# Kernel optimization log

Hardware: AMD Instinct MI355X
Metric: run time of the kernel (lower is better)

## Reference

```python
import jax, jax.numpy as jnp
import numpy as np

N, K = 50000, 16          # nodes, fixed neighbor-list length
IN, HID, OUT = 11, 64, 1  # temporal feat dim, hidden, output


def setup_inputs() -> dict:
    key = jax.random.key(0)
    ks = iter(jax.random.split(key, 64))
    def rn(shape, scale=1.0):
        return jax.random.normal(next(ks), shape, dtype=jnp.float32) * scale
    inp = {
        "x": rn((N, IN)),
        "neighbors": jax.random.randint(next(ks), (N, K), 0, N, dtype=jnp.int32),
        "prev_hidden": rn((N, HID)),
    }
    # DGL SAGEConv(lstm): LSTM(in=d, hid=d), fc_self Linear(d,o,bias=True), fc_neigh Linear(d,o,bias=False)
    dims = [(IN, HID), (HID, HID), (HID, HID), (HID, OUT)]
    for li, (d, o) in enumerate(dims, start=1):
        s = 1.0 / np.sqrt(d)
        inp[f"l{li}_Wih"] = rn((4 * d, d), s)
        inp[f"l{li}_Whh"] = rn((4 * d, d), s)
        inp[f"l{li}_bih"] = rn((4 * d,), s)
        inp[f"l{li}_bhh"] = rn((4 * d,), s)
        inp[f"l{li}_Ws"] = rn((o, d), s)
        inp[f"l{li}_bs"] = rn((o,), s)
        inp[f"l{li}_Wn"] = rn((o, d), s)
    sg = 1.0 / np.sqrt(HID)
    inp["g_Wih"] = rn((3 * HID, HID), sg)
    inp["g_Whh"] = rn((3 * HID, HID), sg)
    inp["g_bih"] = rn((3 * HID,), sg)
    inp["g_bhh"] = rn((3 * HID,), sg)
    return inp


def _sage_conv(h, neighbors, Wih, Whh, bih, bhh, Ws, bs, Wn):
    """DGL SAGEConv with aggregator_type='lstm'."""
    m = h[neighbors]             # [N, K, D] gathered neighbor messages
    ms = jnp.swapaxes(m, 0, 1)   # [K, N, D] time-major for scan
    Nn, D = h.shape
    h0 = jnp.zeros((Nn, D), h.dtype)

    def step(carry, mt):
        hp, cp = carry
        g = mt @ Wih.T + bih + hp @ Whh.T + bhh   # [N, 4D]
        i, f, gg, o = jnp.split(g, 4, axis=-1)    # torch LSTM gate order i,f,g,o
        c = jax.nn.sigmoid(f) * cp + jax.nn.sigmoid(i) * jnp.tanh(gg)
        hn = jax.nn.sigmoid(o) * jnp.tanh(c)
        return (hn, c), None

    (hK, _), _ = jax.lax.scan(step, (h0, h0), ms)  # final hidden state = neighbor agg
    return h @ Ws.T + bs + hK @ Wn.T


def _gru(x, h, Wih, Whh, bih, bhh):
    """torch.nn.GRUCell, gate order r,z,n."""
    gi = x @ Wih.T + bih
    gh = h @ Whh.T + bhh
    ir, iz, inn = jnp.split(gi, 3, axis=-1)
    hr, hz, hn = jnp.split(gh, 3, axis=-1)
    r = jax.nn.sigmoid(ir + hr)
    z = jax.nn.sigmoid(iz + hz)
    n = jnp.tanh(inn + r * hn)
    return (1.0 - z) * n + z * h


def reference(x, neighbors, prev_hidden,
              l1_Wih, l1_Whh, l1_bih, l1_bhh, l1_Ws, l1_bs, l1_Wn,
              l2_Wih, l2_Whh, l2_bih, l2_bhh, l2_Ws, l2_bs, l2_Wn,
              l3_Wih, l3_Whh, l3_bih, l3_bhh, l3_Ws, l3_bs, l3_Wn,
              l4_Wih, l4_Whh, l4_bih, l4_bhh, l4_Ws, l4_bs, l4_Wn,
              g_Wih, g_Whh, g_bih, g_bhh):
    h = jax.nn.relu(_sage_conv(x, neighbors, l1_Wih, l1_Whh, l1_bih, l1_bhh, l1_Ws, l1_bs, l1_Wn))
    h = jax.nn.relu(_sage_conv(h, neighbors, l2_Wih, l2_Whh, l2_bih, l2_bhh, l2_Ws, l2_bs, l2_Wn))
    h = jax.nn.relu(_sage_conv(h, neighbors, l3_Wih, l3_Whh, l3_bih, l3_bhh, l3_Ws, l3_bs, l3_Wn))
    h = _gru(h, prev_hidden, g_Wih, g_Whh, g_bih, g_bhh)
    logits = _sage_conv(h, neighbors, l4_Wih, l4_Whh, l4_bih, l4_bhh, l4_Ws, l4_bs, l4_Wn)
    return logits
```

## Files before the change

### kernel.cpp

```cpp
#include <hip/hip_runtime.h>

#define N_NODES 50000

typedef __bf16 bf16x8 __attribute__((ext_vector_type(8)));
typedef float f32x4 __attribute__((ext_vector_type(4)));

union U16x8 { uint4 v; unsigned short u[8]; bf16x8 b; };

__device__ __forceinline__ float b2f(unsigned short h){
  unsigned int u = ((unsigned int)h) << 16;
  return __builtin_bit_cast(float, u);
}
__device__ __forceinline__ unsigned short f2b(float x){
  unsigned int u = __builtin_bit_cast(unsigned int, x);
  u = u + 0x7FFFu + ((u >> 16) & 1u);
  return (unsigned short)(u >> 16);
}
__device__ __forceinline__ float sigm(float x){
  const float e = __builtin_amdgcn_exp2f(x * -1.4426950408889634f);
  return __builtin_amdgcn_rcpf(1.0f + e);
}
__device__ __forceinline__ float tanh_(float x){
  const float e = __builtin_amdgcn_exp2f(x * 2.8853900817779268f);
  return fmaf(-2.0f, __builtin_amdgcn_rcpf(1.0f + e), 1.0f);
}

__device__ __forceinline__ bf16x8 load8_bf16(const float* p){
  float4 a = *(const float4*)p; float4 c = *(const float4*)(p + 4);
  U16x8 r;
  r.u[0]=f2b(a.x); r.u[1]=f2b(a.y); r.u[2]=f2b(a.z); r.u[3]=f2b(a.w);
  r.u[4]=f2b(c.x); r.u[5]=f2b(c.y); r.u[6]=f2b(c.z); r.u[7]=f2b(c.w);
  return r.b;
}


__global__ __launch_bounds__(256) void l1_kernel(
    const float* __restrict__ x, const int* __restrict__ nbr,
    const float* __restrict__ Wih, const float* __restrict__ Whh,
    const float* __restrict__ bih, const float* __restrict__ bhh,
    const float* __restrict__ Ws,  const float* __restrict__ bs,
    const float* __restrict__ Wn,  unsigned short* __restrict__ out_hl)
{
  __shared__ unsigned short mbuf[16][2][16][24];
  __shared__ unsigned short hbuf[2][2][16][24];
  __shared__ float pre[4][16][17];

  const int tid  = threadIdx.x;
  const int wave = tid >> 6, lane = tid & 63;
  const int n16  = lane & 15, q = lane >> 4;
  const int nb0  = blockIdx.x * 16;

  { unsigned int* p = (unsigned int*)hbuf;
    for (int i = tid; i < 768; i += 256) p[i] = 0u; }

  {
    const int nd = tid >> 4, t = tid & 15;
    const int gn = nbr[(nb0 + nd) * 16 + t];
    const float* row = x + (long)gn * 11;
    float v[16];
    #pragma unroll
    for (int j = 0; j < 11; j++) v[j] = row[j];
    #pragma unroll
    for (int j = 11; j < 16; j++) v[j] = 0.f;
    #pragma unroll
    for (int j = 0; j < 16; j++){
      unsigned short hb = f2b(v[j]);
      mbuf[t][0][nd][j] = hb;
      mbuf[t][1][nd][j] = f2b(v[j] - b2f(hb));
    }
  }

  bf16x8 wf;
  {
    const int u = n16;
    const float* src = (q < 2) ? (Wih + (wave * 11 + u) * 11)
                               : (Whh + (wave * 11 + u) * 11);
    const int kb = (q & 1) * 8;
    U16x8 a;
    #pragma unroll
    for (int j = 0; j < 8; j++){
      const int k = kb + j;
      float v = (u < 11 && k < 11) ? src[k] : 0.f;
      a.u[j] = f2b(v);
    }
    wf = a.b;
  }
  const float bg = (n16 < 11) ? (bih[wave * 11 + n16] + bhh[wave * 11 + n16]) : 0.f;

  const int nd_o = tid & 15, u_o = tid >> 4;
  float c_o = 0.f;

  __syncthreads();

  for (int t = 0; t < 16; t++){
    const int db = t & 1, nb = db ^ 1;

    const unsigned short* ph = (q < 2) ? &mbuf[t][0][n16][q * 8]
                                       : &hbuf[db][0][n16][(q - 2) * 8];
    U16x8 ah, al;
    ah.v = *(const uint4*)ph;
    al.v = *(const uint4*)(ph + 384);

    f32x4 acc = {bg, bg, bg, bg};
    acc = __builtin_amdgcn_mfma_f32_16x16x32_bf16(ah.b, wf, acc, 0, 0, 0);
    acc = __builtin_amdgcn_mfma_f32_16x16x32_bf16(al.b, wf, acc, 0, 0, 0);

    #pragma unroll
    for (int r = 0; r < 4; r++) pre[wave][q * 4 + r][n16] = acc[r];
    __syncthreads();

    if (tid < 176){
      const float gi = pre[0][nd_o][u_o];
      const float gf = pre[1][nd_o][u_o];
      const float gg = pre[2][nd_o][u_o];
      const float go = pre[3][nd_o][u_o];
      c_o = sigm(gf) * c_o + sigm(gi) * tanh_(gg);
      const float hv = sigm(go) * tanh_(c_o);
      const unsigned short hb = f2b(hv);
      hbuf[nb][0][nd_o][u_o] = hb;
      hbuf[nb][1][nd_o][u_o] = f2b(hv - b2f(hb));
    }
    __syncthreads();
  }

  U16x8 eah, eal;
  if (q < 2){
    const float* row = x + (long)(nb0 + n16) * 11;
    U16x8 H, L;
    #pragma unroll
    for (int j = 0; j < 8; j++){
      const int k = q * 8 + j;
      float v = (k < 11) ? row[k] : 0.f;
      unsigned short hb = f2b(v); H.u[j] = hb; L.u[j] = f2b(v - b2f(hb));
    }
    eah = H; eal = L;
  } else {
    const unsigned short* ph = &hbuf[0][0][n16][(q - 2) * 8];
    eah.v = *(const uint4*)ph;
    eal.v = *(const uint4*)(ph + 384);
  }

  bf16x8 ewf;
  {
    const int uo = wave * 16 + n16;
    const float* src = (q < 2) ? (Ws + uo * 11) : (Wn + uo * 11);
    const int kb = (q & 1) * 8;
    U16x8 a;
    #pragma unroll
    for (int j = 0; j < 8; j++){
      const int k = kb + j;
      a.u[j] = f2b((k < 11) ? src[k] : 0.f);
    }
    ewf = a.b;
  }

  {
    const int uo = wave * 16 + n16;
    const float bsv = bs[uo];
    f32x4 e = {bsv, bsv, bsv, bsv};
    e = __builtin_amdgcn_mfma_f32_16x16x32_bf16(eah.b, ewf, e, 0, 0, 0);
    e = __builtin_amdgcn_mfma_f32_16x16x32_bf16(eal.b, ewf, e, 0, 0, 0);
    #pragma unroll
    for (int r = 0; r < 4; r++){
      const float vv = fmaxf(e[r], 0.f);
      const unsigned short hb = f2b(vv);
      const size_t base = (size_t)(nb0 + q * 4 + r) * 128;
      out_hl[base + uo]      = hb;
      out_hl[base + 64 + uo] = f2b(vv - b2f(hb));
    }
  }
}

__global__ __launch_bounds__(256, 3) void sage64_kernel(
    const unsigned short* __restrict__ in_hl, const int* __restrict__ nbr,
    const float* __restrict__ Wih, const float* __restrict__ Whh,
    const float* __restrict__ bih, const float* __restrict__ bhh,
    const float* __restrict__ Ws,  const float* __restrict__ bs,
    const float* __restrict__ Wn,
    unsigned short* __restrict__ out_hl, float* __restrict__ out_f32, int mode)
{
  __shared__ uint4 mbuf[2][16][17];
  __shared__ uint4 hbuf[2][16][17];
  __shared__ int nbr_s[16 * 17];

  const int tid = threadIdx.x;
  const int wv = tid >> 6, lane = tid & 63;
  const int n16 = lane & 15, q = lane >> 4;
  const int nb0 = blockIdx.x * 16;

  { const int nd = tid >> 4, t = tid & 15;
    nbr_s[nd * 17 + t] = nbr[(nb0 + nd) * 16 + t]; }

  { unsigned int* p = (unsigned int*)&hbuf[0][0][0];
    for (int i = tid; i < 1088; i += 256) p[i] = 0u; }

  { const int nd = tid >> 4, s = tid & 15;
    const int gn = nbr[(nb0 + nd) * 16 + 0];
    mbuf[0][nd][s] = *(const uint4*)(in_hl + (size_t)gn * 128 + s * 8); }

  bf16x8 wih_f[4][2], whh_f[4][2];
  #pragma unroll
  for (int g = 0; g < 4; g++){
    const int row = g * 64 + wv * 16 + n16;
    #pragma unroll
    for (int kc = 0; kc < 2; kc++){
      wih_f[g][kc] = load8_bf16(Wih + row * 64 + kc * 32 + q * 8);
      whh_f[g][kc] = load8_bf16(Whh + row * 64 + kc * 32 + q * 8);
    }
  }
  f32x4 bg[4];
  #pragma unroll
  for (int g = 0; g < 4; g++){
    float4 bi = *(const float4*)(bih + g * 64 + wv * 16 + q * 4);
    float4 bh = *(const float4*)(bhh + g * 64 + wv * 16 + q * 4);
    f32x4 s = {bi.x + bh.x, bi.y + bh.y, bi.z + bh.z, bi.w + bh.w};
    bg[g] = s;
  }

  float c4[4] = {0.f, 0.f, 0.f, 0.f};
  __syncthreads();

  for (int t = 0; t < 16; t++){
    const int db = t & 1, nbf = db ^ 1;

    bf16x8 mh[2], ml[2], hh[2], hl[2];
    #pragma unroll
    for (int kc = 0; kc < 2; kc++){
      U16x8 a; a.v = mbuf[db][n16][kc * 4 + q];     mh[kc] = a.b;
      U16x8 b_; b_.v = mbuf[db][n16][8 + kc * 4 + q]; ml[kc] = b_.b;
      U16x8 c_; c_.v = hbuf[db][n16][kc * 4 + q];     hh[kc] = c_.b;
      U16x8 d_; d_.v = hbuf[db][n16][8 + kc * 4 + q]; hl[kc] = d_.b;
    }

    uint4 gv = make_uint4(0u, 0u, 0u, 0u);
    const int nd = tid >> 4, s = tid & 15;
    if (t < 15){
      const int gn = nbr_s[nd * 17 + t + 1];
      gv = *(const uint4*)(in_hl + (size_t)gn * 128 + s * 8);
    }

    f32x4 acc[4];
    #pragma unroll
    for (int g = 0; g < 4; g++) acc[g] = bg[g];
    #pragma unroll
    for (int kc = 0; kc < 2; kc++){
      #pragma unroll
      for (int g = 0; g < 4; g++)
        acc[g] = __builtin_amdgcn_mfma_f32_16x16x32_bf16(wih_f[g][kc], mh[kc], acc[g], 0, 0, 0);
      #pragma unroll
      for (int g = 0; g < 4; g++)
        acc[g] = __builtin_amdgcn_mfma_f32_16x16x32_bf16(wih_f[g][kc], ml[kc], acc[g], 0, 0, 0);
      #pragma unroll
      for (int g = 0; g < 4; g++)
        acc[g] = __builtin_amdgcn_mfma_f32_16x16x32_bf16(whh_f[g][kc], hh[kc], acc[g], 0, 0, 0);
      #pragma unroll
      for (int g = 0; g < 4; g++)
        acc[g] = __builtin_amdgcn_mfma_f32_16x16x32_bf16(whh_f[g][kc], hl[kc], acc[g], 0, 0, 0);
    }

    unsigned short hB[4], lB[4];
    #pragma unroll
    for (int r = 0; r < 4; r++){
      const float iv = sigm(acc[0][r]);
      const float fv = sigm(acc[1][r]);
      const float gg = tanh_(acc[2][r]);
      const float ov = sigm(acc[3][r]);
      c4[r] = fv * c4[r] + iv * gg;
      const float hv = ov * tanh_(c4[r]);
      hB[r] = f2b(hv);
      lB[r] = f2b(hv - b2f(hB[r]));
    }
    {
      uint2* hrow = (uint2*)&hbuf[nbf][n16][0];
      hrow[wv * 4 + q]      = make_uint2((unsigned)hB[0] | ((unsigned)hB[1] << 16),
                                         (unsigned)hB[2] | ((unsigned)hB[3] << 16));
      hrow[16 + wv * 4 + q] = make_uint2((unsigned)lB[0] | ((unsigned)lB[1] << 16),
                                         (unsigned)lB[2] | ((unsigned)lB[3] << 16));
    }
    if (t < 15) mbuf[nbf][nd][s] = gv;
    __syncthreads();
  }

  bf16x8 sH[2], sL[2], kH[2], kL[2];
  #pragma unroll
  for (int kc = 0; kc < 2; kc++){
    U16x8 a; a.v = *(const uint4*)(in_hl + (size_t)(nb0 + n16) * 128 + kc * 32 + q * 8);
    sH[kc] = a.b;
    U16x8 b_; b_.v = *(const uint4*)(in_hl + (size_t)(nb0 + n16) * 128 + 64 + kc * 32 + q * 8);
    sL[kc] = b_.b;
    U16x8 c_; c_.v = hbuf[0][n16][kc * 4 + q];     kH[kc] = c_.b;
    U16x8 d_; d_.v = hbuf[0][n16][8 + kc * 4 + q]; kL[kc] = d_.b;
  }

  if (mode == 0){
    bf16x8 ws_f[2], wn_f[2];
    #pragma unroll
    for (int kc = 0; kc < 2; kc++){
      ws_f[kc] = load8_bf16(Ws + (wv * 16 + n16) * 64 + kc * 32 + q * 8);
      wn_f[kc] = load8_bf16(Wn + (wv * 16 + n16) * 64 + kc * 32 + q * 8);
    }
    float4 bsv = *(const float4*)(bs + wv * 16 + q * 4);
    f32x4 e = {bsv.x, bsv.y, bsv.z, bsv.w};
    #pragma unroll
    for (int kc = 0; kc < 2; kc++){
      e = __builtin_amdgcn_mfma_f32_16x16x32_bf16(ws_f[kc], sH[kc], e, 0, 0, 0);
      e = __builtin_amdgcn_mfma_f32_16x16x32_bf16(ws_f[kc], sL[kc], e, 0, 0, 0);
      e = __builtin_amdgcn_mfma_f32_16x16x32_bf16(wn_f[kc], kH[kc], e, 0, 0, 0);
      e = __builtin_amdgcn_mfma_f32_16x16x32_bf16(wn_f[kc], kL[kc], e, 0, 0, 0);
    }
    unsigned short hB[4], lB[4];
    #pragma unroll
    for (int r = 0; r < 4; r++){
      const float vv = fmaxf(e[r], 0.f);
      hB[r] = f2b(vv);
      lB[r] = f2b(vv - b2f(hB[r]));
    }
    uint2* orow = (uint2*)(out_hl + (size_t)(nb0 + n16) * 128);
    orow[wv * 4 + q]      = make_uint2((unsigned)hB[0] | ((unsigned)hB[1] << 16),
                                       (unsigned)hB[2] | ((unsigned)hB[3] << 16));
    orow[16 + wv * 4 + q] = make_uint2((unsigned)lB[0] | ((unsigned)lB[1] << 16),
                                       (unsigned)lB[2] | ((unsigned)lB[3] << 16));
  } else {
    if (wv == 0){
      bf16x8 ws_f[2], wn_f[2];
      #pragma unroll
      for (int kc = 0; kc < 2; kc++){
        U16x8 a, b_;
        a.v = make_uint4(0u,0u,0u,0u); b_.v = make_uint4(0u,0u,0u,0u);
        if (n16 == 0){
          a.b  = load8_bf16(Ws + kc * 32 + q * 8);
          b_.b = load8_bf16(Wn + kc * 32 + q * 8);
        }
        ws_f[kc] = a.b; wn_f[kc] = b_.b;
      }
      f32x4 e = {0.f, 0.f, 0.f, 0.f};
      #pragma unroll
      for (int kc = 0; kc < 2; kc++){
        e = __builtin_amdgcn_mfma_f32_16x16x32_bf16(ws_f[kc], sH[kc], e, 0, 0, 0);
        e = __builtin_amdgcn_mfma_f32_16x16x32_bf16(ws_f[kc], sL[kc], e, 0, 0, 0);
        e = __builtin_amdgcn_mfma_f32_16x16x32_bf16(wn_f[kc], kH[kc], e, 0, 0, 0);
        e = __builtin_amdgcn_mfma_f32_16x16x32_bf16(wn_f[kc], kL[kc], e, 0, 0, 0);
      }
      if (q == 0) out_f32[nb0 + n16] = e[0] + bs[0];
    }
  }
}

__global__ __launch_bounds__(256) void gru_kernel(
    const unsigned short* __restrict__ h3_hl, const float* __restrict__ prev,
    const float* __restrict__ gWih, const float* __restrict__ gWhh,
    const float* __restrict__ gbih, const float* __restrict__ gbhh,
    unsigned short* __restrict__ out_hl)
{
  const int tid = threadIdx.x, wave = tid >> 6, lane = tid & 63;
  const int n16 = lane & 15, q = lane >> 4;
  const int nb0 = blockIdx.x * 16;
  const int u_ = wave * 16 + n16;

  bf16x8 ah[2], al[2], ap[2];
  #pragma unroll
  for (int kc = 0; kc < 2; kc++){
    U16x8 a; a.v = *(const uint4*)(h3_hl + (size_t)(nb0 + n16) * 128 + kc * 32 + q * 8);
    ah[kc] = a.b;
    U16x8 b_; b_.v = *(const uint4*)(h3_hl + (size_t)(nb0 + n16) * 128 + 64 + kc * 32 + q * 8);
    al[kc] = b_.b;
    ap[kc] = load8_bf16(prev + (size_t)(nb0 + n16) * 64 + kc * 32 + q * 8);
  }

  bf16x8 wi_f[3][2], wh_f[3][2];
  #pragma unroll
  for (int g = 0; g < 3; g++){
    const int row = g * 64 + wave * 16 + n16;
    #pragma unroll
    for (int kc = 0; kc < 2; kc++){
      wi_f[g][kc] = load8_bf16(gWih + row * 64 + kc * 32 + q * 8);
      wh_f[g][kc] = load8_bf16(gWhh + row * 64 + kc * 32 + q * 8);
    }
  }

  f32x4 gi[3], gh[3];
  #pragma unroll
  for (int g = 0; g < 3; g++){
    const float bi = gbih[g * 64 + u_], bh = gbhh[g * 64 + u_];
    f32x4 vi = {bi, bi, bi, bi}; gi[g] = vi;
    f32x4 vh = {bh, bh, bh, bh}; gh[g] = vh;
  }
  #pragma unroll
  for (int kc = 0; kc < 2; kc++){
    #pragma unroll
    for (int g = 0; g < 3; g++)
      gi[g] = __builtin_amdgcn_mfma_f32_16x16x32_bf16(ah[kc], wi_f[g][kc], gi[g], 0, 0, 0);
    #pragma unroll
    for (int g = 0; g < 3; g++)
      gi[g] = __builtin_amdgcn_mfma_f32_16x16x32_bf16(al[kc], wi_f[g][kc], gi[g], 0, 0, 0);
    #pragma unroll
    for (int g = 0; g < 3; g++)
      gh[g] = __builtin_amdgcn_mfma_f32_16x16x32_bf16(ap[kc], wh_f[g][kc], gh[g], 0, 0, 0);
  }

  #pragma unroll
  for (int r = 0; r < 4; r++){
    const long node = nb0 + q * 4 + r;
    const float rv = sigm(gi[0][r] + gh[0][r]);
    const float zv = sigm(gi[1][r] + gh[1][r]);
    const float nv = tanh_(gi[2][r] + rv * gh[2][r]);
    const float hp = prev[node * 64 + u_];
    const float v = (1.f - zv) * nv + zv * hp;
    const unsigned short hb = f2b(v);
    out_hl[(size_t)node * 128 + u_]      = hb;
    out_hl[(size_t)node * 128 + 64 + u_] = f2b(v - b2f(hb));
  }
}

extern "C" void kernel_launch(void* const* d_in, const int* in_sizes, int n_in,
                              void* d_out, int out_size, void* d_ws, size_t ws_size,
                              hipStream_t stream)
{
  (void)in_sizes; (void)n_in; (void)out_size; (void)ws_size;
  const float* x    = (const float*)d_in[0];
  const int*   nbr  = (const int*)d_in[1];
  const float* prev = (const float*)d_in[2];
  auto W = [&](int i){ return (const float*)d_in[i]; };

  unsigned short* tabA = (unsigned short*)d_ws;
  unsigned short* tabB = tabA + (size_t)N_NODES * 128;

  l1_kernel<<<N_NODES / 16, 256, 0, stream>>>(
      x, nbr, W(3), W(4), W(5), W(6), W(7), W(8), W(9), tabA);
  sage64_kernel<<<N_NODES / 16, 256, 0, stream>>>(
      tabA, nbr, W(10), W(11), W(12), W(13), W(14), W(15), W(16), tabB, nullptr, 0);
  sage64_kernel<<<N_NODES / 16, 256, 0, stream>>>(
      tabB, nbr, W(17), W(18), W(19), W(20), W(21), W(22), W(23), tabA, nullptr, 0);
  gru_kernel<<<N_NODES / 16, 256, 0, stream>>>(
      tabA, prev, W(31), W(32), W(33), W(34), tabB);
  sage64_kernel<<<N_NODES / 16, 256, 0, stream>>>(
      tabB, nbr, W(24), W(25), W(26), W(27), W(28), W(29), W(30),
      nullptr, (float*)d_out, 1);
}
```

Before: 598.5 us.

## Drop bf16 hi/lo split activations, prefetch all neighbors to LDS up front

Stores intermediate activations as a single bf16 value instead of a hi+lo bf16 pair, which halves gather traffic and halves the number of MFMAs per LSTM step and in the GRU and projection stages. The sage64 kernel now loads all 16 neighbor rows into shared memory with an XOR-style swizzle before the recurrence, replacing the per-step double-buffered gather. Occupancy hint rises from 3 to 4 blocks. Accuracy drops because the lo correction term is gone, which may exceed tolerance for the deep LSTM chain.

```diff
diff --git a/kernel.cpp b/kernel.cpp
--- a/kernel.cpp
+++ b/kernel.cpp
@@ -163,15 +163,12 @@
     #pragma unroll
     for (int r = 0; r < 4; r++){
       const float vv = fmaxf(e[r], 0.f);
-      const unsigned short hb = f2b(vv);
-      const size_t base = (size_t)(nb0 + q * 4 + r) * 128;
-      out_hl[base + uo]      = hb;
-      out_hl[base + 64 + uo] = f2b(vv - b2f(hb));
-    }
-  }
-}
-
-__global__ __launch_bounds__(256, 3) void sage64_kernel(
+      out_hl[(size_t)(nb0 + q * 4 + r) * 64 + uo] = f2b(vv);
+    }
+  }
+}
+
+__global__ __launch_bounds__(256, 4) void sage64_kernel(
     const unsigned short* __restrict__ in_hl, const int* __restrict__ nbr,
     const float* __restrict__ Wih, const float* __restrict__ Whh,
     const float* __restrict__ bih, const float* __restrict__ bhh,
@@ -179,24 +176,24 @@
     const float* __restrict__ Wn,
     unsigned short* __restrict__ out_hl, float* __restrict__ out_f32, int mode)
 {
-  __shared__ uint4 mbuf[2][16][17];
-  __shared__ uint4 hbuf[2][16][17];
-  __shared__ int nbr_s[16 * 17];
+  __shared__ uint4 mbuf[16][16][8];
+  __shared__ uint4 hbuf[2][16][8];
 
   const int tid = threadIdx.x;
   const int wv = tid >> 6, lane = tid & 63;
   const int n16 = lane & 15, q = lane >> 4;
   const int nb0 = blockIdx.x * 16;
 
-  { const int nd = tid >> 4, t = tid & 15;
-    nbr_s[nd * 17 + t] = nbr[(nb0 + nd) * 16 + t]; }
-
+  {
+    const int nd = tid >> 4, t = tid & 15;
+    const int gn = nbr[(nb0 + nd) * 16 + t];
+    const uint4* src = (const uint4*)(in_hl + (size_t)gn * 64);
+    #pragma unroll
+    for (int s = 0; s < 8; s++)
+      mbuf[t][nd][(s + nd + t) & 7] = src[s];
+  }
   { unsigned int* p = (unsigned int*)&hbuf[0][0][0];
-    for (int i = tid; i < 1088; i += 256) p[i] = 0u; }
-
-  { const int nd = tid >> 4, s = tid & 15;
-    const int gn = nbr[(nb0 + nd) * 16 + 0];
-    mbuf[0][nd][s] = *(const uint4*)(in_hl + (size_t)gn * 128 + s * 8); }
+    for (int i = tid; i < 512; i += 256) p[i] = 0u; }
 
   bf16x8 wih_f[4][2], whh_f[4][2];
   #pragma unroll
@@ -223,20 +220,11 @@
   for (int t = 0; t < 16; t++){
     const int db = t & 1, nbf = db ^ 1;
 
-    bf16x8 mh[2], ml[2], hh[2], hl[2];
-    #pragma unroll
-    for (int kc = 0; kc < 2; kc++){
-      U16x8 a; a.v = mbuf[db][n16][kc * 4 + q];     mh[kc] = a.b;
-      U16x8 b_; b_.v = mbuf[db][n16][8 + kc * 4 + q]; ml[kc] = b_.b;
-      U16x8 c_; c_.v = hbuf[db][n16][kc * 4 + q];     hh[kc] = c_.b;
-      U16x8 d_; d_.v = hbuf[db][n16][8 + kc * 4 + q]; hl[kc] = d_.b;
-    }
-
-    uint4 gv = make_uint4(0u, 0u, 0u, 0u);
-    const int nd = tid >> 4, s = tid & 15;
-    if (t < 15){
-      const int gn = nbr_s[nd * 17 + t + 1];
-      gv = *(const uint4*)(in_hl + (size_t)gn * 128 + s * 8);
+    bf16x8 mh[2], hh[2];
+    #pragma unroll
+    for (int kc = 0; kc < 2; kc++){
+      U16x8 a; a.v = mbuf[t][n16][(kc * 4 + q + n16 + t) & 7]; mh[kc] = a.b;
+      U16x8 c_; c_.v = hbuf[db][n16][(kc * 4 + q + n16) & 7];  hh[kc] = c_.b;
     }
 
     f32x4 acc[4];
@@ -249,16 +237,10 @@
         acc[g] = __builtin_amdgcn_mfma_f32_16x16x32_bf16(wih_f[g][kc], mh[kc], acc[g], 0, 0, 0);
       #pragma unroll
       for (int g = 0; g < 4; g++)
-        acc[g] = __builtin_amdgcn_mfma_f32_16x16x32_bf16(wih_f[g][kc], ml[kc], acc[g], 0, 0, 0);
-      #pragma unroll
-      for (int g = 0; g < 4; g++)
         acc[g] = __builtin_amdgcn_mfma_f32_16x16x32_bf16(whh_f[g][kc], hh[kc], acc[g], 0, 0, 0);
-      #pragma unroll
-      for (int g = 0; g < 4; g++)
-        acc[g] = __builtin_amdgcn_mfma_f32_16x16x32_bf16(whh_f[g][kc], hl[kc], acc[g], 0, 0, 0);
-    }
-
-    unsigned short hB[4], lB[4];
+    }
+
+    unsigned short hB[4];
     #pragma unroll
     for (int r = 0; r < 4; r++){
       const float iv = sigm(acc[0][r]);
@@ -266,30 +248,24 @@
       const float gg = tanh_(acc[2][r]);
       const float ov = sigm(acc[3][r]);
       c4[r] = fv * c4[r] + iv * gg;
-      const float hv = ov * tanh_(c4[r]);
-      hB[r] = f2b(hv);
-      lB[r] = f2b(hv - b2f(hB[r]));
+      hB[r] = f2b(ov * tanh_(c4[r]));
     }
     {
-      uint2* hrow = (uint2*)&hbuf[nbf][n16][0];
-      hrow[wv * 4 + q]      = make_uint2((unsigned)hB[0] | ((unsigned)hB[1] << 16),
-                                         (unsigned)hB[2] | ((unsigned)hB[3] << 16));
-      hrow[16 + wv * 4 + q] = make_uint2((unsigned)lB[0] | ((unsigned)lB[1] << 16),
-                                         (unsigned)lB[2] | ((unsigned)lB[3] << 16));
-    }
-    if (t < 15) mbuf[nbf][nd][s] = gv;
+      const int idx = wv * 4 + q;
+      const int slot = idx >> 1, half = idx & 1;
+      ((uint2*)&hbuf[nbf][n16][(slot + n16) & 7])[half] =
+          make_uint2((unsigned)hB[0] | ((unsigned)hB[1] << 16),
+                     (unsigned)hB[2] | ((unsigned)hB[3] << 16));
+    }
     __syncthreads();
   }
 
-  bf16x8 sH[2], sL[2], kH[2], kL[2];
+  bf16x8 sH[2], kH[2];
   #pragma unroll
   for (int kc = 0; kc < 2; kc++){
-    U16x8 a; a.v = *(const uint4*)(in_hl + (size_t)(nb0 + n16) * 128 + kc * 32 + q * 8);
+    U16x8 a; a.v = *(const uint4*)(in_hl + (size_t)(nb0 + n16) * 64 + kc * 32 + q * 8);
     sH[kc] = a.b;
-    U16x8 b_; b_.v = *(const uint4*)(in_hl + (size_t)(nb0 + n16) * 128 + 64 + kc * 32 + q * 8);
-    sL[kc] = b_.b;
-    U16x8 c_; c_.v = hbuf[0][n16][kc * 4 + q];     kH[kc] = c_.b;
-    U16x8 d_; d_.v = hbuf[0][n16][8 + kc * 4 + q]; kL[kc] = d_.b;
+    U16x8 c_; c_.v = hbuf[0][n16][(kc * 4 + q + n16) & 7]; kH[kc] = c_.b;
   }
 
   if (mode == 0){
@@ -304,22 +280,14 @@
     #pragma unroll
     for (int kc = 0; kc < 2; kc++){
       e = __builtin_amdgcn_mfma_f32_16x16x32_bf16(ws_f[kc], sH[kc], e, 0, 0, 0);
-      e = __builtin_amdgcn_mfma_f32_16x16x32_bf16(ws_f[kc], sL[kc], e, 0, 0, 0);
       e = __builtin_amdgcn_mfma_f32_16x16x32_bf16(wn_f[kc], kH[kc], e, 0, 0, 0);
-      e = __builtin_amdgcn_mfma_f32_16x16x32_bf16(wn_f[kc], kL[kc], e, 0, 0, 0);
-    }
-    unsigned short hB[4], lB[4];
-    #pragma unroll
-    for (int r = 0; r < 4; r++){
-      const float vv = fmaxf(e[r], 0.f);
-      hB[r] = f2b(vv);
-      lB[r] = f2b(vv - b2f(hB[r]));
-    }
-    uint2* orow = (uint2*)(out_hl + (size_t)(nb0 + n16) * 128);
-    orow[wv * 4 + q]      = make_uint2((unsigned)hB[0] | ((unsigned)hB[1] << 16),
-                                       (unsigned)hB[2] | ((unsigned)hB[3] << 16));
-    orow[16 + wv * 4 + q] = make_uint2((unsigned)lB[0] | ((unsigned)lB[1] << 16),
-                                       (unsigned)lB[2] | ((unsigned)lB[3] << 16));
+    }
+    unsigned short oB[4];
+    #pragma unroll
+    for (int r = 0; r < 4; r++) oB[r] = f2b(fmaxf(e[r], 0.f));
+    *(uint2*)(out_hl + (size_t)(nb0 + n16) * 64 + wv * 16 + q * 4) =
+        make_uint2((unsigned)oB[0] | ((unsigned)oB[1] << 16),
+                   (unsigned)oB[2] | ((unsigned)oB[3] << 16));
   } else {
     if (wv == 0){
       bf16x8 ws_f[2], wn_f[2];
@@ -337,9 +305,7 @@
       #pragma unroll
       for (int kc = 0; kc < 2; kc++){
         e = __builtin_amdgcn_mfma_f32_16x16x32_bf16(ws_f[kc], sH[kc], e, 0, 0, 0);
-        e = __builtin_amdgcn_mfma_f32_16x16x32_bf16(ws_f[kc], sL[kc], e, 0, 0, 0);
         e = __builtin_amdgcn_mfma_f32_16x16x32_bf16(wn_f[kc], kH[kc], e, 0, 0, 0);
-        e = __builtin_amdgcn_mfma_f32_16x16x32_bf16(wn_f[kc], kL[kc], e, 0, 0, 0);
       }
       if (q == 0) out_f32[nb0 + n16] = e[0] + bs[0];
     }
@@ -357,13 +323,11 @@
   const int nb0 = blockIdx.x * 16;
   const int u_ = wave * 16 + n16;
 
-  bf16x8 ah[2], al[2], ap[2];
+  bf16x8 ah[2], ap[2];
   #pragma unroll
   for (int kc = 0; kc < 2; kc++){
-    U16x8 a; a.v = *(const uint4*)(h3_hl + (size_t)(nb0 + n16) * 128 + kc * 32 + q * 8);
+    U16x8 a; a.v = *(const uint4*)(h3_hl + (size_t)(nb0 + n16) * 64 + kc * 32 + q * 8);
     ah[kc] = a.b;
-    U16x8 b_; b_.v = *(const uint4*)(h3_hl + (size_t)(nb0 + n16) * 128 + 64 + kc * 32 + q * 8);
-    al[kc] = b_.b;
     ap[kc] = load8_bf16(prev + (size_t)(nb0 + n16) * 64 + kc * 32 + q * 8);
   }
 
@@ -390,9 +354,6 @@
     #pragma unroll
     for (int g = 0; g < 3; g++)
       gi[g] = __builtin_amdgcn_mfma_f32_16x16x32_bf16(ah[kc], wi_f[g][kc], gi[g], 0, 0, 0);
-    #pragma unroll
-    for (int g = 0; g < 3; g++)
-      gi[g] = __builtin_amdgcn_mfma_f32_16x16x32_bf16(al[kc], wi_f[g][kc], gi[g], 0, 0, 0);
     #pragma unroll
     for (int g = 0; g < 3; g++)
       gh[g] = __builtin_amdgcn_mfma_f32_16x16x32_bf16(ap[kc], wh_f[g][kc], gh[g], 0, 0, 0);
@@ -406,9 +367,7 @@
     const float nv = tanh_(gi[2][r] + rv * gh[2][r]);
     const float hp = prev[node * 64 + u_];
     const float v = (1.f - zv) * nv + zv * hp;
-    const unsigned short hb = f2b(v);
-    out_hl[(size_t)node * 128 + u_]      = hb;
-    out_hl[(size_t)node * 128 + 64 + u_] = f2b(v - b2f(hb));
+    out_hl[(size_t)node * 64 + u_] = f2b(v);
   }
 }
 
@@ -423,7 +382,7 @@
   auto W = [&](int i){ return (const float*)d_in[i]; };
 
   unsigned short* tabA = (unsigned short*)d_ws;
-  unsigned short* tabB = tabA + (size_t)N_NODES * 128;
+  unsigned short* tabB = tabA + (size_t)N_NODES * 64;
 
   l1_kernel<<<N_NODES / 16, 256, 0, stream>>>(
       x, nbr, W(3), W(4), W(5), W(6), W(7), W(8), W(9), tabA);
```

New measurement: 591.7 us. About the same (-1.1%).
